# Kernel optimization log

Measured on AMD Instinct MI355X. Metric: run time of the kernel, lower is better.

The kernel has to match this reference:

```python
import jax, jax.numpy as jnp
import numpy as np

TAU = 2.0        # LIFNode tau
ALPHA = 4.0      # spikingjelly default surrogate Sigmoid alpha
EPS = 1e-5       # BatchNorm eps
NUM_HEADS = 8

@jax.custom_vjp
def spike(u):
    # Heaviside with sigmoid surrogate gradient (spikingjelly default)
    return (u >= 0.0).astype(u.dtype)

def _spike_fwd(u):
    return spike(u), u

def _spike_bwd(u, g):
    s = jax.nn.sigmoid(ALPHA * u)
    return (g * ALPHA * s * (1.0 - s),)

spike.defvjp(_spike_fwd, _spike_bwd)

def lif(x, vth=1.0):
    # single-step LIF from rest (v=0, v_reset=0, decay_input=True): v = x / tau
    return spike(x / TAU - vth)

def conv1x1_bn(x, w, gamma, beta, mean, var):
    # 1x1 conv (no bias) + eval-mode BatchNorm, fused affine
    y = jnp.einsum('oc,bchw->bohw', w, x)
    inv = gamma / jnp.sqrt(var + EPS)
    return y * inv[None, :, None, None] + (beta - mean * inv)[None, :, None, None]


def setup_inputs() -> dict:
    B, C, H, W = 16, 768, 32, 32
    key = jax.random.key(0)
    ks = jax.random.split(key, 22)
    def bn(i):
        return (jax.random.uniform(ks[i], (C,)) + 0.5,
                0.1 * jax.random.normal(ks[i + 1], (C,)),
                0.1 * jax.random.normal(ks[i + 2], (C,)),
                jax.random.uniform(ks[i + 3], (C,)) + 0.5)
    q_gamma, q_beta, q_mean, q_var = bn(1)
    k_gamma, k_beta, k_mean, k_var = bn(5)
    v_gamma, v_beta, v_mean, v_var = bn(9)
    p_gamma, p_beta, p_mean, p_var = bn(13)
    W_SCALE = 0.25  # keeps post-BN activations spanning the LIF threshold
    return {
        'x': 3.0 * jax.random.normal(ks[0], (B, C, H, W), dtype=jnp.float32),
        'wq': W_SCALE * jax.random.normal(ks[17], (C, C), dtype=jnp.float32),
        'q_gamma': q_gamma, 'q_beta': q_beta, 'q_mean': q_mean, 'q_var': q_var,
        'wk': W_SCALE * jax.random.normal(ks[18], (C, C), dtype=jnp.float32),
        'k_gamma': k_gamma, 'k_beta': k_beta, 'k_mean': k_mean, 'k_var': k_var,
        'wv': W_SCALE * jax.random.normal(ks[19], (C, C), dtype=jnp.float32),
        'v_gamma': v_gamma, 'v_beta': v_beta, 'v_mean': v_mean, 'v_var': v_var,
        'wp': W_SCALE * jax.random.normal(ks[20], (C, C), dtype=jnp.float32),
        'bp': 0.1 * jax.random.normal(ks[21], (C,), dtype=jnp.float32),
        'p_gamma': p_gamma, 'p_beta': p_beta, 'p_mean': p_mean, 'p_var': p_var,
    }


def reference(x, wq, q_gamma, q_beta, q_mean, q_var,
              wk, k_gamma, k_beta, k_mean, k_var,
              wv, v_gamma, v_beta, v_mean, v_var,
              wp, bp, p_gamma, p_beta, p_mean, p_var):
    B, C, H, W = x.shape
    N = H * W
    h = NUM_HEADS
    hd = C // h
    identity = x
    xs = lif(x)  # shortcut_lif

    def branch(w, g, b, m, vv):
        y = lif(conv1x1_bn(xs, w, g, b, m, vv))            # [B,C,H,W] binary spikes
        y = y.reshape(B, C, N).transpose(0, 2, 1)           # [B,N,C]
        return y.reshape(B, N, h, hd).transpose(0, 2, 1, 3)  # [B,h,N,hd]

    q = branch(wq, q_gamma, q_beta, q_mean, q_var)
    k = branch(wk, k_gamma, k_beta, k_mean, k_var)
    v = branch(wv, v_gamma, v_beta, v_mean, v_var)

    kv = jnp.sum(k * v, axis=2, keepdims=True)  # [B,h,1,hd] token reduction
    kv = lif(kv, vth=0.5)                       # attn_lif

    out = q * kv                                          # [B,h,N,hd]
    out = out.transpose(0, 2, 1, 3).reshape(B, N, C)      # [B,N,C]
    out = out.transpose(0, 2, 1).reshape(B, C, H, W)      # [B,C,H,W]

    y = jnp.einsum('oc,bchw->bohw', wp, out) + bp[None, :, None, None]
    inv = p_gamma / jnp.sqrt(p_var + EPS)
    y = y * inv[None, :, None, None] + (p_beta - p_mean * inv)[None, :, None, None]
    return y + identity
```

## Files before the change

### kernel.cpp

```cpp
#include <hip/hip_runtime.h>
#include <cstdint>
#include <cstddef>

#define C_DIM 768
#define NPIX  1024
#define B_DIM 16
#define NTOT  16384
#define KT_N  12
#define MT_N  6
#define JT_N  128
#define JT2_N 64
#define MT2_N 12
#define TAU   2.0e-3f
#define BCAP  64
#define NBLK  (3 * MT2_N * JT2_N)
#define PLANE_B (C_DIM * C_DIM)
#define TILE_B  8192
#define PREP_SPIKE_BLKS (JT_N * KT_N)
#define PREP_W_BLKS     576
#define PREP_BN_BLKS    12

typedef __attribute__((ext_vector_type(4)))  int   int4v;
typedef __attribute__((ext_vector_type(16))) char  char16v;

__device__ __forceinline__ void gload16(const void* g, void* l) {
    __builtin_amdgcn_global_load_lds(
        (const __attribute__((address_space(1))) unsigned int*)g,
        (__attribute__((address_space(3))) unsigned int*)l, 16, 0, 0);
}

__global__ __launch_bounds__(256) void prep_all(
    const float* __restrict__ x,
    const float* __restrict__ w0, const float* __restrict__ w1,
    const float* __restrict__ w2, const float* __restrict__ w3,
    const float* __restrict__ qg, const float* __restrict__ qb,
    const float* __restrict__ qm, const float* __restrict__ qv,
    const float* __restrict__ kg, const float* __restrict__ kb,
    const float* __restrict__ km, const float* __restrict__ kv,
    const float* __restrict__ vg, const float* __restrict__ vb,
    const float* __restrict__ vm, const float* __restrict__ vv,
    const float* __restrict__ pg, const float* __restrict__ pb,
    const float* __restrict__ pm, const float* __restrict__ pv,
    char* __restrict__ xs, char* __restrict__ wall,
    float* __restrict__ invt, float* __restrict__ biast)
{
    const int blk = blockIdx.x;
    if (blk < PREP_SPIKE_BLKS) {
        const int jt = blk / KT_N, kt = blk - jt * KT_N;
        const int b  = jt >> 3;
        const int n0 = (jt & 7) * 128;
#pragma unroll
        for (int i = 0; i < 2; ++i) {
            int q = threadIdx.x + i * 256;
            int kgc = q >> 7, col = q & 127;
            char16v sv;
#pragma unroll
            for (int e = 0; e < 16; ++e) {
                float xv = x[((size_t)b * C_DIM + (kt * 64 + kgc * 16 + e)) * NPIX + n0 + col];
                sv[e] = (xv >= 2.0f) ? (char)1 : (char)0;
            }
            *(char16v*)(xs + (size_t)(jt * KT_N + kt) * TILE_B + (size_t)q * 16) = sv;
        }
    } else if (blk < PREP_SPIKE_BLKS + PREP_W_BLKS) {
        int t = (blk - PREP_SPIKE_BLKS) * 256 + threadIdx.x;
        int set = t / (C_DIM * 48);
        int rem = t - set * (C_DIM * 48);
        int o = rem / 48, c16 = rem - (rem / 48) * 48;
        const float* w = set == 0 ? w0 : set == 1 ? w1 : set == 2 ? w2 : w3;
        char* pl = wall + (size_t)set * 2 * PLANE_B;
        char16v H, L;
#pragma unroll
        for (int e = 0; e < 16; ++e) {
            float wv = w[(size_t)o * C_DIM + c16 * 16 + e];
            int w16 = (int)lrintf(wv * 16384.0f);
            w16 = w16 > 32639 ? 32639 : (w16 < -32639 ? -32639 : w16);
            int hi = (w16 + 128) >> 8;
            int lo = w16 - (hi << 8);
            H[e] = (char)hi;
            L[e] = (char)lo;
        }
        int mt = o >> 7, m = o & 127;
        int kt = c16 >> 2, kgc = c16 & 3;
        size_t base = (size_t)(kt * MT_N + mt) * TILE_B + kgc * 2048 + (size_t)m * 16;
        *(char16v*)(pl + base)           = H;
        *(char16v*)(pl + PLANE_B + base) = L;
    } else {
        int i = (blk - PREP_SPIKE_BLKS - PREP_W_BLKS) * 256 + threadIdx.x;
        if (i >= 4 * C_DIM) return;
        int set = i / C_DIM, o = i - set * C_DIM;
        const float* g = set == 0 ? qg : set == 1 ? kg : set == 2 ? vg : pg;
        const float* b = set == 0 ? qb : set == 1 ? kb : set == 2 ? vb : pb;
        const float* m = set == 0 ? qm : set == 1 ? km : set == 2 ? vm : pm;
        const float* v = set == 0 ? qv : set == 1 ? kv : set == 2 ? vv : pv;
        float inv = g[o] / sqrtf(v[o] + 1e-5f);
        invt[i]  = inv;
        biast[i] = b[o] - m[o] * inv;
    }
}

__global__ __launch_bounds__(512, 4) void branch_mfma(
    const char* __restrict__ wall, const char* __restrict__ xsblob,
    const float* __restrict__ invt, const float* __restrict__ biast,
    char* __restrict__ sall,
    unsigned int* __restrict__ cntArr, unsigned int* __restrict__ recsB)
{
    __shared__ char stage[2][24576];
    __shared__ unsigned int lcnt;
    const int jt2 = blockIdx.x, mt = blockIdx.y, z = blockIdx.z;
    const int jt0 = jt2 * 2;
    const int tid = threadIdx.x;
    const int lane = tid & 63, wid = tid >> 6;
    const int wm = wid >> 2, wn = wid & 3;
    const int lr = lane & 15, kgl = lane >> 4;
    const char* wblob = wall + (size_t)z * 2 * PLANE_B;
    char* sblob = sall + (size_t)z * (size_t)C_DIM * NTOT;
    const float* invz  = invt  + z * C_DIM;
    const float* biasz = biast + z * C_DIM;
    const unsigned int blk = ((unsigned)z * MT2_N + mt) * JT2_N + jt2;

    const int mt128 = mt >> 1, mrow = (mt & 1) * 64;
    const int aIdx = tid & 255;
    const size_t aoff_src = (size_t)((tid < 256) ? 0 : PLANE_B)
                          + (aIdx >> 6) * 2048 + (size_t)(mrow + (aIdx & 63)) * 16;

#define STG(buf, ktA) do {                                                     \
        const char* Ab_ = wblob + (size_t)((ktA) * MT_N + mt128) * TILE_B;     \
        const char* B0_ = xsblob + (size_t)(jt0 * KT_N + (ktA)) * TILE_B;      \
        const char* B1_ = xsblob + (size_t)((jt0 + 1) * KT_N + (ktA)) * TILE_B;\
        char* d_ = stage[buf];                                                 \
        gload16(Ab_ + aoff_src,                d_ + tid * 16);                 \
        gload16(B0_ + (size_t)tid * 16,        d_ + 8192 + tid * 16);          \
        gload16(B1_ + (size_t)tid * 16,        d_ + 16384 + tid * 16);         \
    } while (0)

    int4v acch[2][4], accl[2][4];
#pragma unroll
    for (int a = 0; a < 2; ++a)
#pragma unroll
        for (int b2 = 0; b2 < 4; ++b2) {
            acch[a][b2] = (int4v){0, 0, 0, 0};
            accl[a][b2] = (int4v){0, 0, 0, 0};
        }

    STG(0, 0);
    STG(1, 1);
    if (tid == 0) lcnt = 0;
    int cur = 0;
    const int arow = (wm * 32 + lr) * 16;
    const int bbase = 8192 + (wn >> 1) * 8192 + ((wn & 1) * 64) * 16;
    for (int kt = 0; kt < KT_N; ++kt) {
        if (kt + 1 < KT_N) asm volatile("s_waitcnt vmcnt(3)");
        else               asm volatile("s_waitcnt vmcnt(0)");
        __builtin_amdgcn_s_barrier();
        __builtin_amdgcn_sched_barrier(0);
        const char* st = stage[cur];
        int4v ah0 = *(const int4v*)&st[kgl * 1024 + arow];
        int4v ah1 = *(const int4v*)&st[kgl * 1024 + arow + 256];
        int4v al0 = *(const int4v*)&st[4096 + kgl * 1024 + arow];
        int4v al1 = *(const int4v*)&st[4096 + kgl * 1024 + arow + 256];
        int4v bfr[4];
#pragma unroll
        for (int fn = 0; fn < 4; ++fn)
            bfr[fn] = *(const int4v*)&st[bbase + kgl * 2048 + (fn * 16 + lr) * 16];
        __builtin_amdgcn_sched_barrier(0);
        asm volatile("s_waitcnt lgkmcnt(0)");
        __builtin_amdgcn_sched_barrier(0);
        __builtin_amdgcn_s_barrier();
        if (kt + 2 < KT_N) STG(cur, kt + 2);
        __builtin_amdgcn_s_setprio(1);
#pragma unroll
        for (int fn = 0; fn < 4; ++fn) {
            acch[0][fn] = __builtin_amdgcn_mfma_i32_16x16x64_i8(ah0, bfr[fn], acch[0][fn], 0, 0, 0);
            acch[1][fn] = __builtin_amdgcn_mfma_i32_16x16x64_i8(ah1, bfr[fn], acch[1][fn], 0, 0, 0);
            accl[0][fn] = __builtin_amdgcn_mfma_i32_16x16x64_i8(al0, bfr[fn], accl[0][fn], 0, 0, 0);
            accl[1][fn] = __builtin_amdgcn_mfma_i32_16x16x64_i8(al1, bfr[fn], accl[1][fn], 0, 0, 0);
        }
        __builtin_amdgcn_s_setprio(0);
        cur ^= 1;
    }
#undef STG

    const int jtw = jt0 + (wn >> 1);
    const int colb = (wn & 1) * 64;
    unsigned int pk[2][4];
#pragma unroll
    for (int fm = 0; fm < 2; ++fm)
#pragma unroll
        for (int fn = 0; fn < 4; ++fn) {
            unsigned int p = 0;
#pragma unroll
            for (int r = 0; r < 4; ++r) {
                int o = mt * 64 + wm * 32 + fm * 16 + kgl * 4 + r;
                int vi = acch[fm][fn][r] * 256 + accl[fm][fn][r];
                float y = (float)vi * 6.103515625e-05f;
                float ybn = y * invz[o] + biasz[o];
                if (ybn >= 2.0f) p |= (1u << (r * 8));
                if (fabsf(ybn - 2.0f) < TAU) {
                    unsigned int idx = atomicAdd(&lcnt, 1u);
                    if (idx < BCAP) {
                        int j = jtw * 128 + colb + fn * 16 + lr;
                        recsB[(size_t)blk * BCAP + idx] =
                            ((unsigned)z << 24) | ((unsigned)o << 14) | (unsigned)j;
                    }
                }
            }
            pk[fm][fn] = p;
        }

#pragma unroll
    for (int fnPair = 0; fnPair < 2; ++fnPair) {
        unsigned int got[4];
#pragma unroll
        for (int t = 0; t < 4; ++t) {
            int sel = (kgl + t) & 3;
            int sfm = sel >> 1, sfn = (sel & 1) * 2 + fnPair;
            unsigned int send =
                sfm == 0 ? (sfn == 0 ? pk[0][0] : sfn == 1 ? pk[0][1] : sfn == 2 ? pk[0][2] : pk[0][3])
                         : (sfn == 0 ? pk[1][0] : sfn == 1 ? pk[1][1] : sfn == 2 ? pk[1][2] : pk[1][3]);
            int src = (((kgl - t) & 3) << 4) + lr;
            got[t] = (unsigned int)__shfl((int)send, src);
        }
        unsigned int part[4];
#pragma unroll
        for (int j = 0; j < 4; ++j) {
            int tsel = (kgl - j) & 3;
            part[j] = tsel == 0 ? got[0] : tsel == 1 ? got[1]
                    : tsel == 2 ? got[2] : got[3];
        }
        int4v chunk = (int4v){(int)part[0], (int)part[1], (int)part[2], (int)part[3]};
        int kg2 = wm * 2 + (kgl >> 1);
        int col = colb + ((kgl & 1) * 2 + fnPair) * 16 + lr;
        size_t off = (size_t)(jtw * KT_N + mt) * TILE_B + (size_t)kg2 * 2048 + (size_t)col * 16;
        *(int4v*)(sblob + off) = chunk;
    }
    __syncthreads();
    if (tid == 0) {
        unsigned int c = lcnt;
        cntArr[blk] = c > BCAP ? BCAP : c;
    }
}

__global__ __launch_bounds__(256) void fixup(
    const char* __restrict__ xs,
    const float* __restrict__ wq, const float* __restrict__ wk, const float* __restrict__ wv,
    const float* __restrict__ qg, const float* __restrict__ qb, const float* __restrict__ qm, const float* __restrict__ qv,
    const float* __restrict__ kg, const float* __restrict__ kb2, const float* __restrict__ km, const float* __restrict__ kvr,
    const float* __restrict__ vg, const float* __restrict__ vb, const float* __restrict__ vm, const float* __restrict__ vv,
    char* __restrict__ sq, char* __restrict__ sk, char* __restrict__ sv,
    const unsigned int* __restrict__ cntArr, const unsigned int* __restrict__ recsB)
{
#pragma clang fp contract(off)
    __shared__ float cw[4][C_DIM];
    const int lane = threadIdx.x & 63;
    const int wvid = threadIdx.x >> 6;
    const int gwave = blockIdx.x * 4 + wvid;
    const int nwaves = gridDim.x * 4;
    const int npairs = NBLK * BCAP;

    for (int p = gwave; p < npairs; p += nwaves) {
        int slot = p / NBLK;
        int reg  = p - slot * NBLK;
        if ((unsigned)slot >= cntArr[reg]) continue;
        unsigned int rec = recsB[(size_t)reg * BCAP + slot];
        int plane = rec >> 24, o = (rec >> 14) & 1023, j = rec & 16383;
        int jt = j >> 7, col = j & 127;
        const float* w = plane == 0 ? wq : plane == 1 ? wk : wv;
        int base = 0;
#pragma unroll
        for (int cc = 0; cc < 12; ++cc) {
            int c = cc * 64 + lane;
            char s = xs[(size_t)(jt * KT_N + (c >> 6)) * TILE_B
                        + ((c >> 4) & 3) * 2048 + col * 16 + (c & 15)];
            float wvv = w[(size_t)o * C_DIM + c];
            bool act = (s != 0);
            unsigned long long m = __ballot(act);
            int pos = __popcll(m & ((1ull << lane) - 1ull));
            if (act) cw[wvid][base + pos] = wvv;
            base += __popcll(m);
        }
        __builtin_amdgcn_s_waitcnt(0);
        if (lane == 0) {
            float s = 0.0f;
            for (int i = 0; i < base; ++i) s = s + cw[wvid][i];
            const float* g  = plane == 0 ? qg : plane == 1 ? kg : vg;
            const float* be = plane == 0 ? qb : plane == 1 ? kb2 : vb;
            const float* me = plane == 0 ? qm : plane == 1 ? km : vm;
            const float* va = plane == 0 ? qv : plane == 1 ? kvr : vv;
            float invv = g[o] / sqrtf(va[o] + 1e-5f);
            float t1 = me[o] * invv;
            float bias = be[o] - t1;
            float t3 = s * invv;
            float ybn = t3 + bias;
            char spv = (ybn >= 2.0f) ? (char)1 : (char)0;
            char* blob = plane == 0 ? sq : plane == 1 ? sk : sv;
            blob[(size_t)(jt * KT_N + (o >> 6)) * TILE_B
                 + ((o >> 4) & 3) * 2048 + col * 16 + (o & 15)] = spv;
        }
    }
}

__global__ __launch_bounds__(256) void kv_mask_blob(
    const char* __restrict__ sk, const char* __restrict__ sv,
    unsigned char* __restrict__ maskb)
{
    const int kt = blockIdx.x, b = blockIdx.y;
    const int t = threadIdx.x;
    const int kgc = t >> 6;
    const int col0 = (t & 63) * 2;
    __shared__ unsigned int lmask[4][4];
    if (t < 16) lmask[t >> 2][t & 3] = 0;
    __syncthreads();
    uint4 acc = make_uint4(0, 0, 0, 0);
    for (int jti = 0; jti < 8; ++jti) {
        size_t base = (size_t)((b * 8 + jti) * KT_N + kt) * TILE_B + kgc * 2048;
#pragma unroll
        for (int cc = 0; cc < 2; ++cc) {
            uint4 kk = *(const uint4*)(sk + base + (size_t)(col0 + cc) * 16);
            uint4 vv = *(const uint4*)(sv + base + (size_t)(col0 + cc) * 16);
            acc.x |= (kk.x & vv.x); acc.y |= (kk.y & vv.y);
            acc.z |= (kk.z & vv.z); acc.w |= (kk.w & vv.w);
        }
    }
    if (acc.x) atomicOr(&lmask[kgc][0], acc.x);
    if (acc.y) atomicOr(&lmask[kgc][1], acc.y);
    if (acc.z) atomicOr(&lmask[kgc][2], acc.z);
    if (acc.w) atomicOr(&lmask[kgc][3], acc.w);
    __syncthreads();
    if (t < 64) {
        int kg2 = t >> 4, e = t & 15;
        unsigned int dw = lmask[kg2][e >> 2];
        unsigned char byte = (dw >> ((e & 3) * 8)) & 0xFF;
        maskb[(size_t)b * C_DIM + kt * 64 + t] = byte ? 1 : 0;
    }
}

__global__ __launch_bounds__(512, 4) void final_mfma(
    const char* __restrict__ wblob, const char* __restrict__ sqblob,
    const unsigned char* __restrict__ maskb,
    const float* __restrict__ x, const float* __restrict__ bp,
    const float* __restrict__ invt, const float* __restrict__ biast,
    float* __restrict__ out)
{
    __shared__ char stage[2][24576];
    __shared__ char mlds[768];
    const int jt2 = blockIdx.x, mt = blockIdx.y;
    const int jt0 = jt2 * 2;
    const int tid = threadIdx.x;
    const int lane = tid & 63, wid = tid >> 6;
    const int wm = wid >> 2, wn = wid & 3;
    const int lr = lane & 15, kgl = lane >> 4;
    const int b = jt0 >> 3;
    const float* invp  = invt  + 3 * C_DIM;
    const float* biasp = biast + 3 * C_DIM;

    const int mt128 = mt >> 1, mrow = (mt & 1) * 64;
    const int aIdx = tid & 255;
    const size_t aoff_src = (size_t)((tid < 256) ? 0 : PLANE_B)
                          + (aIdx >> 6) * 2048 + (size_t)(mrow + (aIdx & 63)) * 16;

#define STG(buf, ktA) do {                                                     \
        const char* Ab_ = wblob + (size_t)((ktA) * MT_N + mt128) * TILE_B;     \
        const char* B0_ = sqblob + (size_t)(jt0 * KT_N + (ktA)) * TILE_B;      \
        const char* B1_ = sqblob + (size_t)((jt0 + 1) * KT_N + (ktA)) * TILE_B;\
        char* d_ = stage[buf];                                                 \
        gload16(Ab_ + aoff_src,                d_ + tid * 16);                 \
        gload16(B0_ + (size_t)tid * 16,        d_ + 8192 + tid * 16);          \
        gload16(B1_ + (size_t)tid * 16,        d_ + 16384 + tid * 16);         \
    } while (0)

    int4v acch[2][4], accl[2][4];
#pragma unroll
    for (int a = 0; a < 2; ++a)
#pragma unroll
        for (int b2 = 0; b2 < 4; ++b2) {
            acch[a][b2] = (int4v){0, 0, 0, 0};
            accl[a][b2] = (int4v){0, 0, 0, 0};
        }

    if (tid < 48)
        *(int4v*)&mlds[tid * 16] = *(const int4v*)(maskb + (size_t)b * C_DIM + tid * 16);
    STG(0, 0);
    STG(1, 1);
    __syncthreads();
    int cur = 0;
    const int arow = (wm * 32 + lr) * 16;
    const int bbase = 8192 + (wn >> 1) * 8192 + ((wn & 1) * 64) * 16;
    for (int kt = 0; kt < KT_N; ++kt) {
        if (kt + 1 < KT_N) asm volatile("s_waitcnt vmcnt(3)");
        else               asm volatile("s_waitcnt vmcnt(0)");
        __builtin_amdgcn_s_barrier();
        __builtin_amdgcn_sched_barrier(0);
        const char* st = stage[cur];
        int4v ah0 = *(const int4v*)&st[kgl * 1024 + arow];
        int4v ah1 = *(const int4v*)&st[kgl * 1024 + arow + 256];
        int4v al0 = *(const int4v*)&st[4096 + kgl * 1024 + arow];
        int4v al1 = *(const int4v*)&st[4096 + kgl * 1024 + arow + 256];
        int4v mp = *(const int4v*)&mlds[kt * 64 + kgl * 16];
        int4v bfr[4];
#pragma unroll
        for (int fn = 0; fn < 4; ++fn)
            bfr[fn] = *(const int4v*)&st[bbase + kgl * 2048 + (fn * 16 + lr) * 16];
        __builtin_amdgcn_sched_barrier(0);
        asm volatile("s_waitcnt lgkmcnt(0)");
        __builtin_amdgcn_sched_barrier(0);
        __builtin_amdgcn_s_barrier();
        if (kt + 2 < KT_N) STG(cur, kt + 2);
#pragma unroll
        for (int fn = 0; fn < 4; ++fn) bfr[fn] &= mp;
        __builtin_amdgcn_s_setprio(1);
#pragma unroll
        for (int fn = 0; fn < 4; ++fn) {
            acch[0][fn] = __builtin_amdgcn_mfma_i32_16x16x64_i8(ah0, bfr[fn], acch[0][fn], 0, 0, 0);
            acch[1][fn] = __builtin_amdgcn_mfma_i32_16x16x64_i8(ah1, bfr[fn], acch[1][fn], 0, 0, 0);
            accl[0][fn] = __builtin_amdgcn_mfma_i32_16x16x64_i8(al0, bfr[fn], accl[0][fn], 0, 0, 0);
            accl[1][fn] = __builtin_amdgcn_mfma_i32_16x16x64_i8(al1, bfr[fn], accl[1][fn], 0, 0, 0);
        }
        __builtin_amdgcn_s_setprio(0);
        cur ^= 1;
    }
#undef STG

    const int jtw = jt0 + (wn >> 1);
    const int n0 = (jtw & 7) * 128;
    const int colb = (wn & 1) * 64;
#pragma unroll
    for (int fm = 0; fm < 2; ++fm)
#pragma unroll
        for (int fn = 0; fn < 4; ++fn)
#pragma unroll
            for (int r = 0; r < 4; ++r) {
                int p = mt * 64 + wm * 32 + fm * 16 + kgl * 4 + r;
                int nl = colb + fn * 16 + lr;
                int vi = acch[fm][fn][r] * 256 + accl[fm][fn][r];
                float pre = (float)vi * 6.103515625e-05f;
                size_t idx = ((size_t)b * C_DIM + p) * NPIX + n0 + nl;
                out[idx] = (pre + bp[p]) * invp[p] + biasp[p] + x[idx];
            }
}

extern "C" void kernel_launch(void* const* d_in, const int* in_sizes, int n_in,
                              void* d_out, int out_size, void* d_ws, size_t ws_size,
                              hipStream_t stream) {
    const float* x  = (const float*)d_in[0];
    const float* wq = (const float*)d_in[1];
    const float* qg = (const float*)d_in[2];
    const float* qb = (const float*)d_in[3];
    const float* qm = (const float*)d_in[4];
    const float* qv = (const float*)d_in[5];
    const float* wk = (const float*)d_in[6];
    const float* kg = (const float*)d_in[7];
    const float* kb = (const float*)d_in[8];
    const float* km = (const float*)d_in[9];
    const float* kvv= (const float*)d_in[10];
    const float* wv = (const float*)d_in[11];
    const float* vg = (const float*)d_in[12];
    const float* vb = (const float*)d_in[13];
    const float* vm = (const float*)d_in[14];
    const float* vv = (const float*)d_in[15];
    const float* wp = (const float*)d_in[16];
    const float* bp = (const float*)d_in[17];
    const float* pg = (const float*)d_in[18];
    const float* pb = (const float*)d_in[19];
    const float* pm = (const float*)d_in[20];
    const float* pv = (const float*)d_in[21];

    const size_t SPIKE = (size_t)C_DIM * NTOT;
    char* sq  = (char*)d_ws;
    char* sk  = sq + SPIKE;
    char* sv  = sk + SPIKE;
    char* xs  = sv + SPIKE;
    char* wall = xs + SPIKE;
    unsigned char* maskb = (unsigned char*)(wall + (size_t)4 * 2 * PLANE_B);
    unsigned int* cntArr = (unsigned int*)(maskb + 16384);
    unsigned int* recsB  = cntArr + NBLK;
    float* invt  = (float*)(recsB + (size_t)NBLK * BCAP);
    float* biast = invt + 4 * C_DIM;
    char* wpb = wall + (size_t)3 * 2 * PLANE_B;

    prep_all<<<PREP_SPIKE_BLKS + PREP_W_BLKS + PREP_BN_BLKS, 256, 0, stream>>>(
        x, wq, wk, wv, wp,
        qg, qb, qm, qv, kg, kb, km, kvv, vg, vb, vm, vv, pg, pb, pm, pv,
        xs, wall, invt, biast);
    branch_mfma<<<dim3(JT2_N, MT2_N, 3), 512, 0, stream>>>(
        wall, xs, invt, biast, sq, cntArr, recsB);
    fixup<<<2048, 256, 0, stream>>>(xs, wq, wk, wv,
                                    qg, qb, qm, qv, kg, kb, km, kvv, vg, vb, vm, vv,
                                    sq, sk, sv, cntArr, recsB);
    kv_mask_blob<<<dim3(KT_N, B_DIM), 256, 0, stream>>>(sk, sv, maskb);
    final_mfma<<<dim3(JT2_N, MT2_N), 512, 0, stream>>>(
        wpb, sq, maskb, x, bp, invt, biast, (float*)d_out);
}
```

Measured before the change: 148.6 us.

## Retile int8 MFMA GEMMs to 128x128 tiles with 4 waves per block

```diff
diff --git a/kernel.cpp b/kernel.cpp
--- a/kernel.cpp
+++ b/kernel.cpp
@@ -9,11 +9,9 @@
 #define KT_N  12
 #define MT_N  6
 #define JT_N  128
-#define JT2_N 64
-#define MT2_N 12
 #define TAU   2.0e-3f
 #define BCAP  64
-#define NBLK  (3 * MT2_N * JT2_N)
+#define NBLK  (3 * MT_N * JT_N)
 #define PLANE_B (C_DIM * C_DIM)
 #define TILE_B  8192
 #define PREP_SPIKE_BLKS (JT_N * KT_N)
@@ -98,7 +96,7 @@
     }
 }
 
-__global__ __launch_bounds__(512, 4) void branch_mfma(
+__global__ __launch_bounds__(256, 2) void branch_mfma(
     const char* __restrict__ wall, const char* __restrict__ xsblob,
     const float* __restrict__ invt, const float* __restrict__ biast,
     char* __restrict__ sall,
@@ -106,36 +104,32 @@
 {
     __shared__ char stage[2][24576];
     __shared__ unsigned int lcnt;
-    const int jt2 = blockIdx.x, mt = blockIdx.y, z = blockIdx.z;
-    const int jt0 = jt2 * 2;
+    const int jt = blockIdx.x, mt = blockIdx.y, z = blockIdx.z;
     const int tid = threadIdx.x;
     const int lane = tid & 63, wid = tid >> 6;
-    const int wm = wid >> 2, wn = wid & 3;
+    const int wm = wid >> 1, wn = wid & 1;
     const int lr = lane & 15, kgl = lane >> 4;
     const char* wblob = wall + (size_t)z * 2 * PLANE_B;
     char* sblob = sall + (size_t)z * (size_t)C_DIM * NTOT;
     const float* invz  = invt  + z * C_DIM;
     const float* biasz = biast + z * C_DIM;
-    const unsigned int blk = ((unsigned)z * MT2_N + mt) * JT2_N + jt2;
-
-    const int mt128 = mt >> 1, mrow = (mt & 1) * 64;
-    const int aIdx = tid & 255;
-    const size_t aoff_src = (size_t)((tid < 256) ? 0 : PLANE_B)
-                          + (aIdx >> 6) * 2048 + (size_t)(mrow + (aIdx & 63)) * 16;
+    const unsigned int blk = ((unsigned)z * MT_N + mt) * JT_N + jt;
 
 #define STG(buf, ktA) do {                                                     \
-        const char* Ab_ = wblob + (size_t)((ktA) * MT_N + mt128) * TILE_B;     \
-        const char* B0_ = xsblob + (size_t)(jt0 * KT_N + (ktA)) * TILE_B;      \
-        const char* B1_ = xsblob + (size_t)((jt0 + 1) * KT_N + (ktA)) * TILE_B;\
+        const char* Ab_ = wblob + (size_t)((ktA) * MT_N + mt) * TILE_B;        \
+        const char* Bb_ = xsblob + (size_t)(jt * KT_N + (ktA)) * TILE_B;       \
         char* d_ = stage[buf];                                                 \
-        gload16(Ab_ + aoff_src,                d_ + tid * 16);                 \
-        gload16(B0_ + (size_t)tid * 16,        d_ + 8192 + tid * 16);          \
-        gload16(B1_ + (size_t)tid * 16,        d_ + 16384 + tid * 16);         \
+        gload16(Ab_ + (size_t)tid * 16,                  d_ + tid * 16);       \
+        gload16(Ab_ + 4096 + (size_t)tid * 16,           d_ + 4096 + tid * 16);\
+        gload16(Ab_ + PLANE_B + (size_t)tid * 16,        d_ + 8192 + tid * 16);\
+        gload16(Ab_ + PLANE_B + 4096 + (size_t)tid * 16, d_ + 12288 + tid * 16);\
+        gload16(Bb_ + (size_t)tid * 16,                  d_ + 16384 + tid * 16);\
+        gload16(Bb_ + 4096 + (size_t)tid * 16,           d_ + 20480 + tid * 16);\
     } while (0)
 
-    int4v acch[2][4], accl[2][4];
-#pragma unroll
-    for (int a = 0; a < 2; ++a)
+    int4v acch[4][4], accl[4][4];
+#pragma unroll
+    for (int a = 0; a < 4; ++a)
 #pragma unroll
         for (int b2 = 0; b2 < 4; ++b2) {
             acch[a][b2] = (int4v){0, 0, 0, 0};
@@ -146,22 +140,23 @@
     STG(1, 1);
     if (tid == 0) lcnt = 0;
     int cur = 0;
-    const int arow = (wm * 32 + lr) * 16;
-    const int bbase = 8192 + (wn >> 1) * 8192 + ((wn & 1) * 64) * 16;
+    const int arow = (wm * 64 + lr) * 16;
+    const int brow = (wn * 64 + lr) * 16;
     for (int kt = 0; kt < KT_N; ++kt) {
-        if (kt + 1 < KT_N) asm volatile("s_waitcnt vmcnt(3)");
+        if (kt + 1 < KT_N) asm volatile("s_waitcnt vmcnt(6)");
         else               asm volatile("s_waitcnt vmcnt(0)");
         __builtin_amdgcn_s_barrier();
         __builtin_amdgcn_sched_barrier(0);
         const char* st = stage[cur];
-        int4v ah0 = *(const int4v*)&st[kgl * 1024 + arow];
-        int4v ah1 = *(const int4v*)&st[kgl * 1024 + arow + 256];
-        int4v al0 = *(const int4v*)&st[4096 + kgl * 1024 + arow];
-        int4v al1 = *(const int4v*)&st[4096 + kgl * 1024 + arow + 256];
-        int4v bfr[4];
+        int4v ah[4], al[4], bfr[4];
+#pragma unroll
+        for (int fm = 0; fm < 4; ++fm) {
+            ah[fm] = *(const int4v*)&st[kgl * 2048 + arow + fm * 256];
+            al[fm] = *(const int4v*)&st[8192 + kgl * 2048 + arow + fm * 256];
+        }
 #pragma unroll
         for (int fn = 0; fn < 4; ++fn)
-            bfr[fn] = *(const int4v*)&st[bbase + kgl * 2048 + (fn * 16 + lr) * 16];
+            bfr[fn] = *(const int4v*)&st[16384 + kgl * 2048 + brow + fn * 256];
         __builtin_amdgcn_sched_barrier(0);
         asm volatile("s_waitcnt lgkmcnt(0)");
         __builtin_amdgcn_sched_barrier(0);
@@ -169,28 +164,26 @@
         if (kt + 2 < KT_N) STG(cur, kt + 2);
         __builtin_amdgcn_s_setprio(1);
 #pragma unroll
-        for (int fn = 0; fn < 4; ++fn) {
-            acch[0][fn] = __builtin_amdgcn_mfma_i32_16x16x64_i8(ah0, bfr[fn], acch[0][fn], 0, 0, 0);
-            acch[1][fn] = __builtin_amdgcn_mfma_i32_16x16x64_i8(ah1, bfr[fn], acch[1][fn], 0, 0, 0);
-            accl[0][fn] = __builtin_amdgcn_mfma_i32_16x16x64_i8(al0, bfr[fn], accl[0][fn], 0, 0, 0);
-            accl[1][fn] = __builtin_amdgcn_mfma_i32_16x16x64_i8(al1, bfr[fn], accl[1][fn], 0, 0, 0);
-        }
+        for (int fm = 0; fm < 4; ++fm)
+#pragma unroll
+            for (int fn = 0; fn < 4; ++fn) {
+                acch[fm][fn] = __builtin_amdgcn_mfma_i32_16x16x64_i8(ah[fm], bfr[fn], acch[fm][fn], 0, 0, 0);
+                accl[fm][fn] = __builtin_amdgcn_mfma_i32_16x16x64_i8(al[fm], bfr[fn], accl[fm][fn], 0, 0, 0);
+            }
         __builtin_amdgcn_s_setprio(0);
         cur ^= 1;
     }
 #undef STG
 
-    const int jtw = jt0 + (wn >> 1);
-    const int colb = (wn & 1) * 64;
-    unsigned int pk[2][4];
-#pragma unroll
-    for (int fm = 0; fm < 2; ++fm)
+    unsigned int pk[4][4];
+#pragma unroll
+    for (int fm = 0; fm < 4; ++fm)
 #pragma unroll
         for (int fn = 0; fn < 4; ++fn) {
             unsigned int p = 0;
 #pragma unroll
             for (int r = 0; r < 4; ++r) {
-                int o = mt * 64 + wm * 32 + fm * 16 + kgl * 4 + r;
+                int o = mt * 128 + wm * 64 + fm * 16 + kgl * 4 + r;
                 int vi = acch[fm][fn][r] * 256 + accl[fm][fn][r];
                 float y = (float)vi * 6.103515625e-05f;
                 float ybn = y * invz[o] + biasz[o];
@@ -198,7 +191,7 @@
                 if (fabsf(ybn - 2.0f) < TAU) {
                     unsigned int idx = atomicAdd(&lcnt, 1u);
                     if (idx < BCAP) {
-                        int j = jtw * 128 + colb + fn * 16 + lr;
+                        int j = jt * 128 + wn * 64 + fn * 16 + lr;
                         recsB[(size_t)blk * BCAP + idx] =
                             ((unsigned)z << 24) | ((unsigned)o << 14) | (unsigned)j;
                     }
@@ -208,15 +201,13 @@
         }
 
 #pragma unroll
-    for (int fnPair = 0; fnPair < 2; ++fnPair) {
+    for (int fn = 0; fn < 4; ++fn) {
         unsigned int got[4];
 #pragma unroll
         for (int t = 0; t < 4; ++t) {
             int sel = (kgl + t) & 3;
-            int sfm = sel >> 1, sfn = (sel & 1) * 2 + fnPair;
-            unsigned int send =
-                sfm == 0 ? (sfn == 0 ? pk[0][0] : sfn == 1 ? pk[0][1] : sfn == 2 ? pk[0][2] : pk[0][3])
-                         : (sfn == 0 ? pk[1][0] : sfn == 1 ? pk[1][1] : sfn == 2 ? pk[1][2] : pk[1][3]);
+            unsigned int send = sel == 0 ? pk[0][fn] : sel == 1 ? pk[1][fn]
+                              : sel == 2 ? pk[2][fn] : pk[3][fn];
             int src = (((kgl - t) & 3) << 4) + lr;
             got[t] = (unsigned int)__shfl((int)send, src);
         }
@@ -228,9 +219,9 @@
                     : tsel == 2 ? got[2] : got[3];
         }
         int4v chunk = (int4v){(int)part[0], (int)part[1], (int)part[2], (int)part[3]};
-        int kg2 = wm * 2 + (kgl >> 1);
-        int col = colb + ((kgl & 1) * 2 + fnPair) * 16 + lr;
-        size_t off = (size_t)(jtw * KT_N + mt) * TILE_B + (size_t)kg2 * 2048 + (size_t)col * 16;
+        int col = wn * 64 + fn * 16 + lr;
+        size_t off = (size_t)(jt * KT_N + mt * 2 + wm) * TILE_B
+                   + (size_t)kgl * 2048 + (size_t)col * 16;
         *(int4v*)(sblob + off) = chunk;
     }
     __syncthreads();
@@ -334,7 +325,7 @@
     }
 }
 
-__global__ __launch_bounds__(512, 4) void final_mfma(
+__global__ __launch_bounds__(256, 2) void final_mfma(
     const char* __restrict__ wblob, const char* __restrict__ sqblob,
     const unsigned char* __restrict__ maskb,
     const float* __restrict__ x, const float* __restrict__ bp,
@@ -343,34 +334,30 @@
 {
     __shared__ char stage[2][24576];
     __shared__ char mlds[768];
-    const int jt2 = blockIdx.x, mt = blockIdx.y;
-    const int jt0 = jt2 * 2;
+    const int jt = blockIdx.x, mt = blockIdx.y;
     const int tid = threadIdx.x;
     const int lane = tid & 63, wid = tid >> 6;
-    const int wm = wid >> 2, wn = wid & 3;
+    const int wm = wid >> 1, wn = wid & 1;
     const int lr = lane & 15, kgl = lane >> 4;
-    const int b = jt0 >> 3;
+    const int b = jt >> 3;
     const float* invp  = invt  + 3 * C_DIM;
     const float* biasp = biast + 3 * C_DIM;
 
-    const int mt128 = mt >> 1, mrow = (mt & 1) * 64;
-    const int aIdx = tid & 255;
-    const size_t aoff_src = (size_t)((tid < 256) ? 0 : PLANE_B)
-                          + (aIdx >> 6) * 2048 + (size_t)(mrow + (aIdx & 63)) * 16;
-
 #define STG(buf, ktA) do {                                                     \
-        const char* Ab_ = wblob + (size_t)((ktA) * MT_N + mt128) * TILE_B;     \
-        const char* B0_ = sqblob + (size_t)(jt0 * KT_N + (ktA)) * TILE_B;      \
-        const char* B1_ = sqblob + (size_t)((jt0 + 1) * KT_N + (ktA)) * TILE_B;\
+        const char* Ab_ = wblob + (size_t)((ktA) * MT_N + mt) * TILE_B;        \
+        const char* Bb_ = sqblob + (size_t)(jt * KT_N + (ktA)) * TILE_B;       \
         char* d_ = stage[buf];                                                 \
-        gload16(Ab_ + aoff_src,                d_ + tid * 16);                 \
-        gload16(B0_ + (size_t)tid * 16,        d_ + 8192 + tid * 16);          \
-        gload16(B1_ + (size_t)tid * 16,        d_ + 16384 + tid * 16);         \
+        gload16(Ab_ + (size_t)tid * 16,                  d_ + tid * 16);       \
+        gload16(Ab_ + 4096 + (size_t)tid * 16,           d_ + 4096 + tid * 16);\
+        gload16(Ab_ + PLANE_B + (size_t)tid * 16,        d_ + 8192 + tid * 16);\
+        gload16(Ab_ + PLANE_B + 4096 + (size_t)tid * 16, d_ + 12288 + tid * 16);\
+        gload16(Bb_ + (size_t)tid * 16,                  d_ + 16384 + tid * 16);\
+        gload16(Bb_ + 4096 + (size_t)tid * 16,           d_ + 20480 + tid * 16);\
     } while (0)
 
-    int4v acch[2][4], accl[2][4];
-#pragma unroll
-    for (int a = 0; a < 2; ++a)
+    int4v acch[4][4], accl[4][4];
+#pragma unroll
+    for (int a = 0; a < 4; ++a)
 #pragma unroll
         for (int b2 = 0; b2 < 4; ++b2) {
             acch[a][b2] = (int4v){0, 0, 0, 0};
@@ -383,23 +370,24 @@
     STG(1, 1);
     __syncthreads();
     int cur = 0;
-    const int arow = (wm * 32 + lr) * 16;
-    const int bbase = 8192 + (wn >> 1) * 8192 + ((wn & 1) * 64) * 16;
+    const int arow = (wm * 64 + lr) * 16;
+    const int brow = (wn * 64 + lr) * 16;
     for (int kt = 0; kt < KT_N; ++kt) {
-        if (kt + 1 < KT_N) asm volatile("s_waitcnt vmcnt(3)");
+        if (kt + 1 < KT_N) asm volatile("s_waitcnt vmcnt(6)");
         else               asm volatile("s_waitcnt vmcnt(0)");
         __builtin_amdgcn_s_barrier();
         __builtin_amdgcn_sched_barrier(0);
         const char* st = stage[cur];
-        int4v ah0 = *(const int4v*)&st[kgl * 1024 + arow];
-        int4v ah1 = *(const int4v*)&st[kgl * 1024 + arow + 256];
-        int4v al0 = *(const int4v*)&st[4096 + kgl * 1024 + arow];
-        int4v al1 = *(const int4v*)&st[4096 + kgl * 1024 + arow + 256];
+        int4v ah[4], al[4], bfr[4];
+#pragma unroll
+        for (int fm = 0; fm < 4; ++fm) {
+            ah[fm] = *(const int4v*)&st[kgl * 2048 + arow + fm * 256];
+            al[fm] = *(const int4v*)&st[8192 + kgl * 2048 + arow + fm * 256];
+        }
+#pragma unroll
+        for (int fn = 0; fn < 4; ++fn)
+            bfr[fn] = *(const int4v*)&st[16384 + kgl * 2048 + brow + fn * 256];
         int4v mp = *(const int4v*)&mlds[kt * 64 + kgl * 16];
-        int4v bfr[4];
-#pragma unroll
-        for (int fn = 0; fn < 4; ++fn)
-            bfr[fn] = *(const int4v*)&st[bbase + kgl * 2048 + (fn * 16 + lr) * 16];
         __builtin_amdgcn_sched_barrier(0);
         asm volatile("s_waitcnt lgkmcnt(0)");
         __builtin_amdgcn_sched_barrier(0);
@@ -409,28 +397,26 @@
         for (int fn = 0; fn < 4; ++fn) bfr[fn] &= mp;
         __builtin_amdgcn_s_setprio(1);
 #pragma unroll
-        for (int fn = 0; fn < 4; ++fn) {
-            acch[0][fn] = __builtin_amdgcn_mfma_i32_16x16x64_i8(ah0, bfr[fn], acch[0][fn], 0, 0, 0);
-            acch[1][fn] = __builtin_amdgcn_mfma_i32_16x16x64_i8(ah1, bfr[fn], acch[1][fn], 0, 0, 0);
-            accl[0][fn] = __builtin_amdgcn_mfma_i32_16x16x64_i8(al0, bfr[fn], accl[0][fn], 0, 0, 0);
-            accl[1][fn] = __builtin_amdgcn_mfma_i32_16x16x64_i8(al1, bfr[fn], accl[1][fn], 0, 0, 0);
-        }
+        for (int fm = 0; fm < 4; ++fm)
+#pragma unroll
+            for (int fn = 0; fn < 4; ++fn) {
+                acch[fm][fn] = __builtin_amdgcn_mfma_i32_16x16x64_i8(ah[fm], bfr[fn], acch[fm][fn], 0, 0, 0);
+                accl[fm][fn] = __builtin_amdgcn_mfma_i32_16x16x64_i8(al[fm], bfr[fn], accl[fm][fn], 0, 0, 0);
+            }
         __builtin_amdgcn_s_setprio(0);
         cur ^= 1;
     }
 #undef STG
 
-    const int jtw = jt0 + (wn >> 1);
-    const int n0 = (jtw & 7) * 128;
-    const int colb = (wn & 1) * 64;
-#pragma unroll
-    for (int fm = 0; fm < 2; ++fm)
+    const int n0 = (jt & 7) * 128;
+#pragma unroll
+    for (int fm = 0; fm < 4; ++fm)
 #pragma unroll
         for (int fn = 0; fn < 4; ++fn)
 #pragma unroll
             for (int r = 0; r < 4; ++r) {
-                int p = mt * 64 + wm * 32 + fm * 16 + kgl * 4 + r;
-                int nl = colb + fn * 16 + lr;
+                int p = mt * 128 + wm * 64 + fm * 16 + kgl * 4 + r;
+                int nl = wn * 64 + fn * 16 + lr;
                 int vi = acch[fm][fn][r] * 256 + accl[fm][fn][r];
                 float pre = (float)vi * 6.103515625e-05f;
                 size_t idx = ((size_t)b * C_DIM + p) * NPIX + n0 + nl;
@@ -481,12 +467,12 @@
         x, wq, wk, wv, wp,
         qg, qb, qm, qv, kg, kb, km, kvv, vg, vb, vm, vv, pg, pb, pm, pv,
         xs, wall, invt, biast);
-    branch_mfma<<<dim3(JT2_N, MT2_N, 3), 512, 0, stream>>>(
+    branch_mfma<<<dim3(JT_N, MT_N, 3), 256, 0, stream>>>(
         wall, xs, invt, biast, sq, cntArr, recsB);
     fixup<<<2048, 256, 0, stream>>>(xs, wq, wk, wv,
                                     qg, qb, qm, qv, kg, kb, km, kvv, vg, vb, vm, vv,
                                     sq, sk, sv, cntArr, recsB);
     kv_mask_blob<<<dim3(KT_N, B_DIM), 256, 0, stream>>>(sk, sv, maskb);
-    final_mfma<<<dim3(JT2_N, MT2_N), 512, 0, stream>>>(
+    final_mfma<<<dim3(JT_N, MT_N), 256, 0, stream>>>(
         wpb, sq, maskb, x, bp, invt, biast, (float*)d_out);
 }
```

After: 162.4 us. 9.3% more time.

## Process K-tiles in pairs with one barrier pair per two stages

Applied to the files above, without the earlier changes.

```diff
diff --git a/kernel.cpp b/kernel.cpp
--- a/kernel.cpp
+++ b/kernel.cpp
@@ -145,38 +145,53 @@
     STG(0, 0);
     STG(1, 1);
     if (tid == 0) lcnt = 0;
-    int cur = 0;
     const int arow = (wm * 32 + lr) * 16;
     const int bbase = 8192 + (wn >> 1) * 8192 + ((wn & 1) * 64) * 16;
-    for (int kt = 0; kt < KT_N; ++kt) {
-        if (kt + 1 < KT_N) asm volatile("s_waitcnt vmcnt(3)");
-        else               asm volatile("s_waitcnt vmcnt(0)");
+    for (int kp = 0; kp < KT_N; kp += 2) {
+        asm volatile("s_waitcnt vmcnt(0)");
         __builtin_amdgcn_s_barrier();
         __builtin_amdgcn_sched_barrier(0);
-        const char* st = stage[cur];
-        int4v ah0 = *(const int4v*)&st[kgl * 1024 + arow];
-        int4v ah1 = *(const int4v*)&st[kgl * 1024 + arow + 256];
-        int4v al0 = *(const int4v*)&st[4096 + kgl * 1024 + arow];
-        int4v al1 = *(const int4v*)&st[4096 + kgl * 1024 + arow + 256];
-        int4v bfr[4];
+        const char* s0 = stage[0];
+        int4v ah0a = *(const int4v*)&s0[kgl * 1024 + arow];
+        int4v ah1a = *(const int4v*)&s0[kgl * 1024 + arow + 256];
+        int4v al0a = *(const int4v*)&s0[4096 + kgl * 1024 + arow];
+        int4v al1a = *(const int4v*)&s0[4096 + kgl * 1024 + arow + 256];
+        int4v bfa[4];
 #pragma unroll
         for (int fn = 0; fn < 4; ++fn)
-            bfr[fn] = *(const int4v*)&st[bbase + kgl * 2048 + (fn * 16 + lr) * 16];
+            bfa[fn] = *(const int4v*)&s0[bbase + kgl * 2048 + (fn * 16 + lr) * 16];
+        __builtin_amdgcn_s_setprio(1);
+#pragma unroll
+        for (int fn = 0; fn < 4; ++fn) {
+            acch[0][fn] = __builtin_amdgcn_mfma_i32_16x16x64_i8(ah0a, bfa[fn], acch[0][fn], 0, 0, 0);
+            acch[1][fn] = __builtin_amdgcn_mfma_i32_16x16x64_i8(ah1a, bfa[fn], acch[1][fn], 0, 0, 0);
+            accl[0][fn] = __builtin_amdgcn_mfma_i32_16x16x64_i8(al0a, bfa[fn], accl[0][fn], 0, 0, 0);
+            accl[1][fn] = __builtin_amdgcn_mfma_i32_16x16x64_i8(al1a, bfa[fn], accl[1][fn], 0, 0, 0);
+        }
+        __builtin_amdgcn_s_setprio(0);
+        const char* s1 = stage[1];
+        int4v ah0b = *(const int4v*)&s1[kgl * 1024 + arow];
+        int4v ah1b = *(const int4v*)&s1[kgl * 1024 + arow + 256];
+        int4v al0b = *(const int4v*)&s1[4096 + kgl * 1024 + arow];
+        int4v al1b = *(const int4v*)&s1[4096 + kgl * 1024 + arow + 256];
+        int4v bfb[4];
+#pragma unroll
+        for (int fn = 0; fn < 4; ++fn)
+            bfb[fn] = *(const int4v*)&s1[bbase + kgl * 2048 + (fn * 16 + lr) * 16];
         __builtin_amdgcn_sched_barrier(0);
         asm volatile("s_waitcnt lgkmcnt(0)");
         __builtin_amdgcn_sched_barrier(0);
         __builtin_amdgcn_s_barrier();
-        if (kt + 2 < KT_N) STG(cur, kt + 2);
+        if (kp + 2 < KT_N) { STG(0, kp + 2); STG(1, kp + 3); }
         __builtin_amdgcn_s_setprio(1);
 #pragma unroll
         for (int fn = 0; fn < 4; ++fn) {
-            acch[0][fn] = __builtin_amdgcn_mfma_i32_16x16x64_i8(ah0, bfr[fn], acch[0][fn], 0, 0, 0);
-            acch[1][fn] = __builtin_amdgcn_mfma_i32_16x16x64_i8(ah1, bfr[fn], acch[1][fn], 0, 0, 0);
-            accl[0][fn] = __builtin_amdgcn_mfma_i32_16x16x64_i8(al0, bfr[fn], accl[0][fn], 0, 0, 0);
-            accl[1][fn] = __builtin_amdgcn_mfma_i32_16x16x64_i8(al1, bfr[fn], accl[1][fn], 0, 0, 0);
+            acch[0][fn] = __builtin_amdgcn_mfma_i32_16x16x64_i8(ah0b, bfb[fn], acch[0][fn], 0, 0, 0);
+            acch[1][fn] = __builtin_amdgcn_mfma_i32_16x16x64_i8(ah1b, bfb[fn], acch[1][fn], 0, 0, 0);
+            accl[0][fn] = __builtin_amdgcn_mfma_i32_16x16x64_i8(al0b, bfb[fn], accl[0][fn], 0, 0, 0);
+            accl[1][fn] = __builtin_amdgcn_mfma_i32_16x16x64_i8(al1b, bfb[fn], accl[1][fn], 0, 0, 0);
         }
         __builtin_amdgcn_s_setprio(0);
-        cur ^= 1;
     }
 #undef STG
 
@@ -382,41 +397,59 @@
     STG(0, 0);
     STG(1, 1);
     __syncthreads();
-    int cur = 0;
     const int arow = (wm * 32 + lr) * 16;
     const int bbase = 8192 + (wn >> 1) * 8192 + ((wn & 1) * 64) * 16;
-    for (int kt = 0; kt < KT_N; ++kt) {
-        if (kt + 1 < KT_N) asm volatile("s_waitcnt vmcnt(3)");
-        else               asm volatile("s_waitcnt vmcnt(0)");
+    for (int kp = 0; kp < KT_N; kp += 2) {
+        asm volatile("s_waitcnt vmcnt(0)");
         __builtin_amdgcn_s_barrier();
         __builtin_amdgcn_sched_barrier(0);
-        const char* st = stage[cur];
-        int4v ah0 = *(const int4v*)&st[kgl * 1024 + arow];
-        int4v ah1 = *(const int4v*)&st[kgl * 1024 + arow + 256];
-        int4v al0 = *(const int4v*)&st[4096 + kgl * 1024 + arow];
-        int4v al1 = *(const int4v*)&st[4096 + kgl * 1024 + arow + 256];
-        int4v mp = *(const int4v*)&mlds[kt * 64 + kgl * 16];
-        int4v bfr[4];
-#pragma unroll
-        for (int fn = 0; fn < 4; ++fn)
-            bfr[fn] = *(const int4v*)&st[bbase + kgl * 2048 + (fn * 16 + lr) * 16];
+        const char* s0 = stage[0];
+        int4v ah0a = *(const int4v*)&s0[kgl * 1024 + arow];
+        int4v ah1a = *(const int4v*)&s0[kgl * 1024 + arow + 256];
+        int4v al0a = *(const int4v*)&s0[4096 + kgl * 1024 + arow];
+        int4v al1a = *(const int4v*)&s0[4096 + kgl * 1024 + arow + 256];
+        int4v mpa = *(const int4v*)&mlds[kp * 64 + kgl * 16];
+        int4v bfa[4];
+#pragma unroll
+        for (int fn = 0; fn < 4; ++fn) {
+            bfa[fn] = *(const int4v*)&s0[bbase + kgl * 2048 + (fn * 16 + lr) * 16];
+            bfa[fn] &= mpa;
+        }
+        __builtin_amdgcn_s_setprio(1);
+#pragma unroll
+        for (int fn = 0; fn < 4; ++fn) {
+            acch[0][fn] = __builtin_amdgcn_mfma_i32_16x16x64_i8(ah0a, bfa[fn], acch[0][fn], 0, 0, 0);
+            acch[1][fn] = __builtin_amdgcn_mfma_i32_16x16x64_i8(ah1a, bfa[fn], acch[1][fn], 0, 0, 0);
+            accl[0][fn] = __builtin_amdgcn_mfma_i32_16x16x64_i8(al0a, bfa[fn], accl[0][fn], 0, 0, 0);
+            accl[1][fn] = __builtin_amdgcn_mfma_i32_16x16x64_i8(al1a, bfa[fn], accl[1][fn], 0, 0, 0);
+        }
+        __builtin_amdgcn_s_setprio(0);
+        const char* s1 = stage[1];
+        int4v ah0b = *(const int4v*)&s1[kgl * 1024 + arow];
+        int4v ah1b = *(const int4v*)&s1[kgl * 1024 + arow + 256];
+        int4v al0b = *(const int4v*)&s1[4096 + kgl * 1024 + arow];
+        int4v al1b = *(const int4v*)&s1[4096 + kgl * 1024 + arow + 256];
+        int4v mpb = *(const int4v*)&mlds[(kp + 1) * 64 + kgl * 16];
+        int4v bfb[4];
+#pragma unroll
+        for (int fn = 0; fn < 4; ++fn) {
+            bfb[fn] = *(const int4v*)&s1[bbase + kgl * 2048 + (fn * 16 + lr) * 16];
+            bfb[fn] &= mpb;
+        }
         __builtin_amdgcn_sched_barrier(0);
         asm volatile("s_waitcnt lgkmcnt(0)");
         __builtin_amdgcn_sched_barrier(0);
         __builtin_amdgcn_s_barrier();
-        if (kt + 2 < KT_N) STG(cur, kt + 2);
-#pragma unroll
-        for (int fn = 0; fn < 4; ++fn) bfr[fn] &= mp;
+        if (kp + 2 < KT_N) { STG(0, kp + 2); STG(1, kp + 3); }
         __builtin_amdgcn_s_setprio(1);
 #pragma unroll
         for (int fn = 0; fn < 4; ++fn) {
-            acch[0][fn] = __builtin_amdgcn_mfma_i32_16x16x64_i8(ah0, bfr[fn], acch[0][fn], 0, 0, 0);
-            acch[1][fn] = __builtin_amdgcn_mfma_i32_16x16x64_i8(ah1, bfr[fn], acch[1][fn], 0, 0, 0);
-            accl[0][fn] = __builtin_amdgcn_mfma_i32_16x16x64_i8(al0, bfr[fn], accl[0][fn], 0, 0, 0);
-            accl[1][fn] = __builtin_amdgcn_mfma_i32_16x16x64_i8(al1, bfr[fn], accl[1][fn], 0, 0, 0);
+            acch[0][fn] = __builtin_amdgcn_mfma_i32_16x16x64_i8(ah0b, bfb[fn], acch[0][fn], 0, 0, 0);
+            acch[1][fn] = __builtin_amdgcn_mfma_i32_16x16x64_i8(ah1b, bfb[fn], acch[1][fn], 0, 0, 0);
+            accl[0][fn] = __builtin_amdgcn_mfma_i32_16x16x64_i8(al0b, bfb[fn], accl[0][fn], 0, 0, 0);
+            accl[1][fn] = __builtin_amdgcn_mfma_i32_16x16x64_i8(al1b, bfb[fn], accl[1][fn], 0, 0, 0);
         }
         __builtin_amdgcn_s_setprio(0);
-        cur ^= 1;
     }
 #undef STG
 
```

Measured after the change: 150.0 us. No clear change (+0.9%).
